# Performance work log

Measured on AMD Instinct MI355X. Metric: run time of the kernel, lower is better.

## Reference

```python
import jax, jax.numpy as jnp
import numpy as np

HIDDEN = 256
HEADS = 8
HEAD_SIZE = HIDDEN // HEADS  # 32
CTX = 512
FF = 4 * HIDDEN
LN_EPS = 1e-5


def setup_inputs() -> dict:
    key = jax.random.key(0)
    ks = jax.random.split(key, 12)
    s = 0.02
    return {
        "x": jax.random.normal(ks[0], (32, CTX, HIDDEN), dtype=jnp.float32),
        # per-head Q/K/V projections, stored [H, D, E] ([in, out] orientation)
        "wq": jax.random.normal(ks[1], (HEADS, HIDDEN, HEAD_SIZE), dtype=jnp.float32) * s,
        "wk": jax.random.normal(ks[2], (HEADS, HIDDEN, HEAD_SIZE), dtype=jnp.float32) * s,
        "wv": jax.random.normal(ks[3], (HEADS, HIDDEN, HEAD_SIZE), dtype=jnp.float32) * s,
        "w_proj": jax.random.normal(ks[4], (HIDDEN, HIDDEN), dtype=jnp.float32) * s,
        "w1": jax.random.normal(ks[5], (HIDDEN, FF), dtype=jnp.float32) * s,
        "b1": jnp.zeros((FF,), dtype=jnp.float32),
        "w2": jax.random.normal(ks[6], (FF, HIDDEN), dtype=jnp.float32) * s,
        "b2": jnp.zeros((HIDDEN,), dtype=jnp.float32),
        "g_ln1": jnp.ones((HIDDEN,), dtype=jnp.float32),
        "be_ln1": jnp.zeros((HIDDEN,), dtype=jnp.float32),
        "g_ln2": jnp.ones((HIDDEN,), dtype=jnp.float32),
        "be_ln2": jnp.zeros((HIDDEN,), dtype=jnp.float32),
    }


def _layernorm(x, g, b):
    mu = jnp.mean(x, axis=-1, keepdims=True)
    var = jnp.var(x, axis=-1, keepdims=True)
    return (x - mu) * jax.lax.rsqrt(var + LN_EPS) * g + b


def reference(x, wq, wk, wv, w_proj, w1, b1, w2, b2, g_ln1, be_ln1, g_ln2, be_ln2):
    B, S, D = x.shape  # S == CTX
    # per-head projections: [B, H, S, E]
    q = jnp.einsum("bsd,hde->bhse", x, wq)
    k = jnp.einsum("bsd,hde->bhse", x, wk)
    v = jnp.einsum("bsd,hde->bhse", x, wv)
    scores = jnp.einsum("bhse,bhte->bhst", q, k) * (HEAD_SIZE ** -0.5)
    causal = jnp.tril(jnp.ones((S, S), dtype=bool))  # [S, S]
    scores = jnp.where(causal, scores, -jnp.inf)
    attn = jax.nn.softmax(scores, axis=-1)
    ctx = jnp.einsum("bhst,bhte->bhse", attn, v)
    ctx = ctx.transpose(0, 2, 1, 3).reshape(B, S, D)  # concat heads
    attn_out = ctx @ w_proj
    h = x + _layernorm(attn_out, g_ln1, be_ln1)
    ff = jax.nn.relu(h @ w1 + b1) @ w2 + b2
    return x + _layernorm(ff, g_ln2, be_ln2)
```

## Files before the change

kernel.cpp:

```cpp
#include <hip/hip_runtime.h>
#include <hip/hip_bf16.h>

#define B_   32
#define S_   512
#define D_   256
#define H_   8
#define E_   32
#define FF_  1024
#define T_   (B_ * S_)

typedef __attribute__((ext_vector_type(8))) short short8;
typedef __attribute__((ext_vector_type(4))) float f32x4;

static __device__ __forceinline__ unsigned short f2bf(float f) {
    union { float f; unsigned int u; } c; c.f = f;
    unsigned int u = c.u;
    u += 0x7fffu + ((u >> 16) & 1u);
    return (unsigned short)(u >> 16);
}
static __device__ __forceinline__ float bf2f(unsigned short u) {
    union { unsigned int u; float f; } c; c.u = ((unsigned int)u) << 16;
    return c.f;
}
static __device__ __forceinline__ unsigned int cvtpk(float lo, float hi) {
    unsigned int r;
    asm("v_cvt_pk_bf16_f32 %0, %1, %2" : "=v"(r) : "v"(lo), "v"(hi));
    return r;
}

#define GLOAD16(g, l) __builtin_amdgcn_global_load_lds( \
    (const __attribute__((address_space(1))) void*)(g), \
    (__attribute__((address_space(3))) void*)(l), 16, 0, 0)

__global__ void prep_kernel(const float* __restrict__ x,
                            const float* __restrict__ wq, const float* __restrict__ wk,
                            const float* __restrict__ wv, const float* __restrict__ w_proj,
                            const float* __restrict__ w1, const float* __restrict__ w2,
                            unsigned short* __restrict__ xb, unsigned short* __restrict__ Wqkv,
                            unsigned short* __restrict__ Wproj, unsigned short* __restrict__ W1t,
                            unsigned short* __restrict__ W2t) {
    int blk = blockIdx.x, tid = threadIdx.x;
    if (blk < 4096) {
        int i = blk * 256 + tid;
        float4 v = *(const float4*)&x[(size_t)i * 4];
        ushort4 o; o.x = f2bf(v.x); o.y = f2bf(v.y); o.z = f2bf(v.z); o.w = f2bf(v.w);
        *(ushort4*)&xb[(size_t)i * 4] = o;
    } else if (blk < 4864) {
        int idx = (blk - 4096) * 256 + tid;
        int nn = idx >> 8, k = idx & 255;
        int which = nn >> 8, r = nn & 255, h = r >> 5, e = r & 31;
        const float* w = (which == 0) ? wq : (which == 1 ? wk : wv);
        float v = w[(h * D_ + k) * E_ + e];
        if (which == 0) v *= 0.17677669529663687f * 1.4426950408889634f;
        Wqkv[idx] = f2bf(v);
    } else if (blk < 5120) {
        int idx = (blk - 4864) * 256 + tid;
        int nn = idx >> 8, k = idx & 255;
        Wproj[idx] = f2bf(w_proj[(size_t)k * 256 + nn]);
    } else if (blk < 6144) {
        int idx = (blk - 5120) * 256 + tid;
        int nn = idx >> 8, k = idx & 255;
        W1t[idx] = f2bf(w1[(size_t)k * 1024 + nn]);
    } else {
        int idx = (blk - 6144) * 256 + tid;
        int nn = idx >> 10, k = idx & 1023;
        W2t[idx] = f2bf(w2[(size_t)k * 256 + nn]);
    }
}

template <int EP, int BN>
__global__ __launch_bounds__(256) void gemm_mfma(const unsigned short* __restrict__ A,
                                                 const unsigned short* __restrict__ Bt,
                                                 const float* __restrict__ bias,
                                                 void* __restrict__ Cout,
                                                 unsigned short* __restrict__ Vout,
                                                 int M, int N, int K) {
    constexpr int FN = BN / 32;
    constexpr int NLD = 2 + BN / 64;
    __shared__ char smem[24576 + BN * 192];
    const int tid = threadIdx.x;
    const int bm = blockIdx.y * 128, bn = blockIdx.x * BN;
    const int wave = tid >> 6, lane = tid & 63;
    const int l15 = lane & 15, kc = lane >> 4;
    const int wr = (wave >> 1) * 64, wc = (wave & 1) * (BN / 2);

    auto waitN = [&]() {
        if constexpr (NLD == 3)      asm volatile("s_waitcnt vmcnt(3)" ::: "memory");
        else if constexpr (NLD == 4) asm volatile("s_waitcnt vmcnt(4)" ::: "memory");
        else                         asm volatile("s_waitcnt vmcnt(6)" ::: "memory");
    };

    auto stage = [&](int buf, int kt) {
        int k0 = kt * 32;
        char* aBase = smem + buf * 8192;
        char* bBase = smem + 24576 + buf * (BN * 64);
        #pragma unroll
        for (int j = 0; j < 2; ++j) {
            int o = j * 256 + tid;
            int r = o >> 2, c = o & 3;
            int g = c ^ ((r >> 1) & 3);
            GLOAD16(A + (size_t)(bm + r) * K + k0 + g * 8, aBase + o * 16);
        }
        #pragma unroll
        for (int j = 0; j < BN / 64; ++j) {
            int o = j * 256 + tid;
            int r = o >> 2, c = o & 3;
            int g = c ^ ((r >> 1) & 3);
            GLOAD16(Bt + (size_t)(bn + r) * K + k0 + g * 8, bBase + o * 16);
        }
    };

    f32x4 acc[4][FN];
    #pragma unroll
    for (int m = 0; m < 4; ++m)
        #pragma unroll
        for (int n = 0; n < FN; ++n) acc[m][n] = (f32x4){0.f, 0.f, 0.f, 0.f};

    const int NT = K >> 5;
    stage(0, 0);
    stage(1, 1);
    waitN();
    __builtin_amdgcn_s_barrier();

    int cur = 0;
    for (int kt = 0; kt < NT; ++kt) {
        const char* aBase = smem + cur * 8192;
        const char* bBase = smem + 24576 + cur * (BN * 64);
        short8 afr[4], bfr[FN];
        #pragma unroll
        for (int m = 0; m < 4; ++m) {
            int row = wr + m * 16 + l15;
            int cc = kc ^ ((row >> 1) & 3);
            afr[m] = *(const short8*)(aBase + row * 64 + cc * 16);
        }
        #pragma unroll
        for (int n = 0; n < FN; ++n) {
            int row = wc + n * 16 + l15;
            int cc = kc ^ ((row >> 1) & 3);
            bfr[n] = *(const short8*)(bBase + row * 64 + cc * 16);
        }
        int nxt2 = cur + 2; if (nxt2 >= 3) nxt2 -= 3;
        if (kt + 2 < NT) stage(nxt2, kt + 2);

        __builtin_amdgcn_s_setprio(1);
        #pragma unroll
        for (int m = 0; m < 4; ++m)
            #pragma unroll
            for (int n = 0; n < FN; ++n)
                acc[m][n] = __builtin_amdgcn_mfma_f32_16x16x32_bf16(afr[m], bfr[n], acc[m][n], 0, 0, 0);
        __builtin_amdgcn_s_setprio(0);

        if (kt + 1 < NT) {
            if (kt + 2 < NT) waitN();
            else asm volatile("s_waitcnt vmcnt(0)" ::: "memory");
            __builtin_amdgcn_s_barrier();
        }
        ++cur; if (cur >= 3) cur -= 3;
    }

    if (EP & 8) {
        #pragma unroll
        for (int n = 0; n < FN; ++n) {
            int col = bn + wc + n * 16 + l15;
            if (col < 512) {
                #pragma unroll
                for (int m = 0; m < 4; ++m) {
                    int row0 = bm + wr + m * 16 + kc * 4;
                    #pragma unroll
                    for (int j = 0; j < 4; ++j)
                        ((unsigned short*)Cout)[(size_t)(row0 + j) * 512 + col] = f2bf(acc[m][n][j]);
                }
            } else {
                int hh = (col - 512) >> 5, e = (col - 512) & 31;
                #pragma unroll
                for (int m = 0; m < 4; ++m) {
                    int row0 = bm + wr + m * 16 + kc * 4;
                    int bb = row0 >> 9, s0 = row0 & 511;
                    ushort4 o4;
                    o4.x = f2bf(acc[m][n][0]); o4.y = f2bf(acc[m][n][1]);
                    o4.z = f2bf(acc[m][n][2]); o4.w = f2bf(acc[m][n][3]);
                    *(ushort4*)&Vout[(size_t)(bb * 8 + hh) * 16384 + e * 512 + s0] = o4;
                }
            }
        }
    } else {
        #pragma unroll
        for (int n = 0; n < FN; ++n) {
            int col = bn + wc + n * 16 + l15;
            float bv = (EP & 1) ? bias[col] : 0.f;
            #pragma unroll
            for (int m = 0; m < 4; ++m) {
                int row0 = bm + wr + m * 16 + kc * 4;
                #pragma unroll
                for (int j = 0; j < 4; ++j) {
                    float v = acc[m][n][j] + bv;
                    if (EP & 2) v = fmaxf(v, 0.f);
                    if (EP & 4) ((unsigned short*)Cout)[(size_t)(row0 + j) * N + col] = f2bf(v);
                    else        ((float*)Cout)[(size_t)(row0 + j) * N + col] = v;
                }
            }
        }
    }
}

template <int BIAS, int OUTF32>
__global__ __launch_bounds__(256) void gemm_ln2(const unsigned short* __restrict__ A,
                                                const unsigned short* __restrict__ Bt,
                                                const float* __restrict__ bias,
                                                const float* __restrict__ xres,
                                                const float* __restrict__ gw,
                                                const float* __restrict__ bw,
                                                void* __restrict__ Cout,
                                                int K) {
    __shared__ char smem[55296];
    __shared__ float sred[2][2][32];
    const int tid = threadIdx.x;
    const int bm = blockIdx.x * 32;
    const int wave = tid >> 6, lane = tid & 63;
    const int l15 = lane & 15, kc = lane >> 4;
    const int wr = (wave >> 1) * 16, wc = (wave & 1) * 128;

    auto stage = [&](int buf, int kt) {
        int k0 = kt * 32;
        char* aBase = smem + buf * 2048;
        char* bBase = smem + 6144 + buf * 16384;
        {
            int o = tid & 127;
            int r = o >> 2, c = o & 3;
            int g = c ^ ((r >> 1) & 3);
            GLOAD16(A + (size_t)(bm + r) * K + k0 + g * 8, aBase + o * 16);
        }
        #pragma unroll
        for (int j = 0; j < 4; ++j) {
            int o = j * 256 + tid;
            int r = o >> 2, c = o & 3;
            int g = c ^ ((r >> 1) & 3);
            GLOAD16(Bt + (size_t)r * K + k0 + g * 8, bBase + o * 16);
        }
    };

    f32x4 acc[8];
    #pragma unroll
    for (int n = 0; n < 8; ++n) acc[n] = (f32x4){0.f, 0.f, 0.f, 0.f};

    const int NT = K >> 5;
    stage(0, 0);
    stage(1, 1);
    asm volatile("s_waitcnt vmcnt(5)" ::: "memory");
    __builtin_amdgcn_s_barrier();

    int cur = 0;
    for (int kt = 0; kt < NT; ++kt) {
        const char* aBase = smem + cur * 2048;
        const char* bBase = smem + 6144 + cur * 16384;
        short8 afr, bfr[8];
        {
            int row = wr + l15;
            int cc = kc ^ ((row >> 1) & 3);
            afr = *(const short8*)(aBase + row * 64 + cc * 16);
        }
        #pragma unroll
        for (int n = 0; n < 8; ++n) {
            int row = wc + n * 16 + l15;
            int cc = kc ^ ((row >> 1) & 3);
            bfr[n] = *(const short8*)(bBase + row * 64 + cc * 16);
        }
        int nxt2 = cur + 2; if (nxt2 >= 3) nxt2 -= 3;
        if (kt + 2 < NT) stage(nxt2, kt + 2);

        __builtin_amdgcn_s_setprio(1);
        #pragma unroll
        for (int n = 0; n < 8; ++n)
            acc[n] = __builtin_amdgcn_mfma_f32_16x16x32_bf16(afr, bfr[n], acc[n], 0, 0, 0);
        __builtin_amdgcn_s_setprio(0);

        if (kt + 1 < NT) {
            if (kt + 2 < NT) asm volatile("s_waitcnt vmcnt(5)" ::: "memory");
            else             asm volatile("s_waitcnt vmcnt(0)" ::: "memory");
            __builtin_amdgcn_s_barrier();
        }
        ++cur; if (cur >= 3) cur -= 3;
    }

    float gv[8], bev[8];
    #pragma unroll
    for (int n = 0; n < 8; ++n) {
        int col = wc + n * 16 + l15;
        gv[n] = gw[col]; bev[n] = bw[col];
        if (BIAS) {
            float bb = bias[col];
            #pragma unroll
            for (int j = 0; j < 4; ++j) acc[n][j] += bb;
        }
    }

    #pragma unroll
    for (int j = 0; j < 4; ++j) {
        float s = 0.f, s2 = 0.f;
        #pragma unroll
        for (int n = 0; n < 8; ++n) { float v = acc[n][j]; s += v; s2 += v * v; }
        #pragma unroll
        for (int off = 1; off < 16; off <<= 1) {
            s += __shfl_xor(s, off); s2 += __shfl_xor(s2, off);
        }
        if (l15 == 0) {
            int rl = wr + kc * 4 + j;
            sred[wave & 1][0][rl] = s;
            sred[wave & 1][1][rl] = s2;
        }
    }
    __syncthreads();

    #pragma unroll
    for (int j = 0; j < 4; ++j) {
        int rl = wr + kc * 4 + j;
        float stot  = sred[0][0][rl] + sred[1][0][rl];
        float s2tot = sred[0][1][rl] + sred[1][1][rl];
        float mu  = stot * (1.f / 256.f);
        float var = s2tot * (1.f / 256.f) - mu * mu;
        float rr  = rsqrtf(var + 1e-5f);
        int rowg = bm + rl;
        #pragma unroll
        for (int n = 0; n < 8; ++n) {
            int col = wc + n * 16 + l15;
            float o = xres[(size_t)rowg * 256 + col] + (acc[n][j] - mu) * rr * gv[n] + bev[n];
            if (OUTF32) ((float*)Cout)[(size_t)rowg * 256 + col] = o;
            else ((unsigned short*)Cout)[(size_t)rowg * 256 + col] = f2bf(o);
        }
    }
}

__global__ __launch_bounds__(512, 1) void attn_mfma(const unsigned short* __restrict__ qk,
                                                    const unsigned short* __restrict__ vtg,
                                                    unsigned short* __restrict__ ctx) {
    __shared__ unsigned short klds[512 * 32];
    __shared__ unsigned short vlds[32 * 512];
    __shared__ unsigned short plds[8][32 * 64];
    const int bh = blockIdx.x;
    const int b = bh >> 3, h = bh & 7;
    const int tid = threadIdx.x;
    const int wave = tid >> 6, lane = tid & 63;
    const int l15 = lane & 15, kc = lane >> 4;

    const unsigned short* kg = qk + (size_t)b * 512 * 512 + 256 + h * 32;
    #pragma unroll
    for (int it = 0; it < 4; ++it) {
        int slot = it * 512 + tid;
        int r = slot >> 2, c = slot & 3;
        GLOAD16(kg + (size_t)r * 512 + (c ^ ((r >> 1) & 3)) * 8, (char*)klds + slot * 16);
    }
    #pragma unroll
    for (int it = 0; it < 4; ++it) {
        int slot = it * 512 + tid;
        int e = slot >> 6, c = slot & 63;
        GLOAD16(vtg + (size_t)bh * 16384 + e * 512 + (c ^ (e & 7)) * 8,
                (char*)vlds + slot * 16);
    }

    const int cA = wave, cB = 15 - wave;
    const int ntA = (cA >> 1) + 1, ntB = (cB >> 1) + 1;
    short8 qfA[2], qfB[2];
    #pragma unroll
    for (int qm = 0; qm < 2; ++qm) {
        qfA[qm] = *(const short8*)(qk + (size_t)(b * 512 + cA * 32 + qm * 16 + l15) * 512 + h * 32 + kc * 8);
        qfB[qm] = *(const short8*)(qk + (size_t)(b * 512 + cB * 32 + qm * 16 + l15) * 512 + h * 32 + kc * 8);
    }
    __syncthreads();

    unsigned short* pw = plds[wave];
    const int xsw = (l15 & 7) << 1;

    f32x4 OA[2][2], OB[2][2];
    float lA[2] = {0.f, 0.f}, lB[2] = {0.f, 0.f};
    #pragma unroll
    for (int qm = 0; qm < 2; ++qm) {
        OA[qm][0] = (f32x4){0.f, 0.f, 0.f, 0.f}; OA[qm][1] = (f32x4){0.f, 0.f, 0.f, 0.f};
        OB[qm][0] = (f32x4){0.f, 0.f, 0.f, 0.f}; OB[qm][1] = (f32x4){0.f, 0.f, 0.f, 0.f};
    }

    auto chunk_step = [&](const short8* qf, f32x4 (&O)[2][2], float* lreg,
                          int cc_, bool diag, const short8* kf, int t0) {
        #pragma unroll
        for (int qm = 0; qm < 2; ++qm) {
            f32x4 st[4];
            __builtin_amdgcn_s_setprio(1);
            #pragma unroll
            for (int tn = 0; tn < 4; ++tn)
                st[tn] = __builtin_amdgcn_mfma_f32_16x16x32_bf16(kf[tn], qf[qm],
                                                                 (f32x4){0.f, 0.f, 0.f, 0.f}, 0, 0, 0);
            __builtin_amdgcn_s_setprio(0);
            if (diag) {
                int qg = cc_ * 32 + qm * 16 + l15;
                #pragma unroll
                for (int tn = 0; tn < 4; ++tn)
                    #pragma unroll
                    for (int j = 0; j < 4; ++j)
                        if (t0 + tn * 16 + kc * 4 + j > qg) st[tn][j] = -1e30f;
            }
            float psum = 0.f;
            #pragma unroll
            for (int tn = 0; tn < 4; ++tn) {
                float p0 = __builtin_amdgcn_exp2f(st[tn][0]);
                float p1 = __builtin_amdgcn_exp2f(st[tn][1]);
                float p2 = __builtin_amdgcn_exp2f(st[tn][2]);
                float p3 = __builtin_amdgcn_exp2f(st[tn][3]);
                psum += (p0 + p1) + (p2 + p3);
                uint2 w;
                w.x = cvtpk(p0, p1);
                w.y = cvtpk(p2, p3);
                int tc = (tn * 4 + kc) ^ xsw;
                *(uint2*)(pw + (qm * 16 + l15) * 64 + tc * 4) = w;
            }
            psum += __shfl_xor(psum, 16);
            psum += __shfl_xor(psum, 32);
            lreg[qm] += psum;
        }
        #pragma unroll
        for (int tt = 0; tt < 2; ++tt) {
            short8 pa[2];
            #pragma unroll
            for (int qm = 0; qm < 2; ++qm) {
                int tcr = (tt * 8 + kc * 2) ^ xsw;
                pa[qm] = *(const short8*)(pw + (qm * 16 + l15) * 64 + tcr * 4);
            }
            short8 vt[2];
            #pragma unroll
            for (int n = 0; n < 2; ++n) {
                int e = n * 16 + l15;
                int c = ((t0 >> 3) + tt * 4 + kc) ^ (e & 7);
                vt[n] = *(const short8*)(vlds + e * 512 + c * 8);
            }
            __builtin_amdgcn_s_setprio(1);
            #pragma unroll
            for (int qm = 0; qm < 2; ++qm)
                #pragma unroll
                for (int n = 0; n < 2; ++n)
                    O[qm][n] = __builtin_amdgcn_mfma_f32_16x16x32_bf16(pa[qm], vt[n], O[qm][n], 0, 0, 0);
            __builtin_amdgcn_s_setprio(0);
        }
    };

    for (int ti = 0; ti < ntB; ++ti) {
        const int t0 = ti * 64;
        short8 kf[4];
        #pragma unroll
        for (int tn = 0; tn < 4; ++tn) {
            int row = t0 + tn * 16 + l15;
            int cx = kc ^ ((row >> 1) & 3);
            kf[tn] = *(const short8*)((const char*)klds + row * 64 + cx * 16);
        }
        if (ti < ntA) chunk_step(qfA, OA, lA, cA, ti == ntA - 1, kf, t0);
        chunk_step(qfB, OB, lB, cB, ti == ntB - 1, kf, t0);
    }

    auto epilogue = [&](f32x4 (&O)[2][2], float* lreg, int cc_) {
        #pragma unroll
        for (int qm = 0; qm < 2; ++qm) {
            float linv = 1.f / lreg[qm];
            #pragma unroll
            for (int j = 0; j < 4; ++j) {
                float lj = __shfl(linv, kc * 4 + j, 16);
                size_t base = (size_t)(b * 512 + cc_ * 32 + qm * 16 + kc * 4 + j) * 256 + h * 32;
                ctx[base + l15]      = f2bf(O[qm][0][j] * lj);
                ctx[base + 16 + l15] = f2bf(O[qm][1][j] * lj);
            }
        }
    };
    epilogue(OA, lA, cA);
    epilogue(OB, lB, cB);
}

extern "C" void kernel_launch(void* const* d_in, const int* in_sizes, int n_in,
                              void* d_out, int out_size, void* d_ws, size_t ws_size,
                              hipStream_t stream) {
    (void)in_sizes; (void)n_in; (void)out_size; (void)ws_size;
    const float* x      = (const float*)d_in[0];
    const float* wq     = (const float*)d_in[1];
    const float* wk     = (const float*)d_in[2];
    const float* wv     = (const float*)d_in[3];
    const float* w_proj = (const float*)d_in[4];
    const float* w1     = (const float*)d_in[5];
    const float* b1     = (const float*)d_in[6];
    const float* w2     = (const float*)d_in[7];
    const float* b2     = (const float*)d_in[8];
    const float* g1     = (const float*)d_in[9];
    const float* be1    = (const float*)d_in[10];
    const float* g2     = (const float*)d_in[11];
    const float* be2    = (const float*)d_in[12];
    float* out = (float*)d_out;

    char* W = (char*)d_ws;
    unsigned short* qk      = (unsigned short*)(W + 0);
    unsigned short* vtg     = (unsigned short*)(W + 16777216);
    unsigned short* xb      = (unsigned short*)(W + 25165824);
    unsigned short* ctx     = (unsigned short*)(W + 25165824);
    unsigned short* hbuf    = (unsigned short*)(W + 33554432);
    unsigned short* ff1     = (unsigned short*)(W + 0);
    unsigned short* Wqkv_t  = (unsigned short*)(W + 50331648);
    unsigned short* Wproj_t = (unsigned short*)(W + 50724864);
    unsigned short* W1_t    = (unsigned short*)(W + 50855936);
    unsigned short* W2_t    = (unsigned short*)(W + 51380224);

    prep_kernel<<<7168, 256, 0, stream>>>(x, wq, wk, wv, w_proj, w1, w2,
                                          xb, Wqkv_t, Wproj_t, W1_t, W2_t);

    gemm_mfma<8, 128><<<dim3(6, T_ / 128), 256, 0, stream>>>(xb, Wqkv_t, nullptr, qk, vtg, T_, 768, 256);

    attn_mfma<<<B_ * H_, 512, 0, stream>>>(qk, vtg, ctx);

    gemm_ln2<0, 0><<<T_ / 32, 256, 0, stream>>>(ctx, Wproj_t, nullptr, x, g1, be1, hbuf, 256);

    gemm_mfma<7, 256><<<dim3(FF_ / 256, T_ / 128), 256, 0, stream>>>(hbuf, W1_t, b1, ff1, nullptr, T_, FF_, 256);

    gemm_ln2<1, 1><<<T_ / 32, 256, 0, stream>>>(ff1, W2_t, b2, x, g2, be2, out, 1024);
}
```

Before: 102.7 us.

## Widen MFMA GEMM blocks to 8 waves with 256-row tiles

```diff
diff --git a/kernel.cpp b/kernel.cpp
--- a/kernel.cpp
+++ b/kernel.cpp
@@ -69,44 +69,52 @@
 }
 
 template <int EP, int BN>
-__global__ __launch_bounds__(256) void gemm_mfma(const unsigned short* __restrict__ A,
-                                                 const unsigned short* __restrict__ Bt,
-                                                 const float* __restrict__ bias,
-                                                 void* __restrict__ Cout,
-                                                 unsigned short* __restrict__ Vout,
-                                                 int M, int N, int K) {
+__global__ __launch_bounds__(512, 2) void gemm_mfma8(const unsigned short* __restrict__ A,
+                                                     const unsigned short* __restrict__ Bt,
+                                                     const float* __restrict__ bias,
+                                                     void* __restrict__ Cout,
+                                                     unsigned short* __restrict__ Vout,
+                                                     int M, int N, int K) {
     constexpr int FN = BN / 32;
-    constexpr int NLD = 2 + BN / 64;
-    __shared__ char smem[24576 + BN * 192];
+    __shared__ char smem[49152 + BN * 192];
     const int tid = threadIdx.x;
-    const int bm = blockIdx.y * 128, bn = blockIdx.x * BN;
+    const int bm = blockIdx.y * 256, bn = blockIdx.x * BN;
     const int wave = tid >> 6, lane = tid & 63;
     const int l15 = lane & 15, kc = lane >> 4;
-    const int wr = (wave >> 1) * 64, wc = (wave & 1) * (BN / 2);
-
-    auto waitN = [&]() {
-        if constexpr (NLD == 3)      asm volatile("s_waitcnt vmcnt(3)" ::: "memory");
-        else if constexpr (NLD == 4) asm volatile("s_waitcnt vmcnt(4)" ::: "memory");
-        else                         asm volatile("s_waitcnt vmcnt(6)" ::: "memory");
-    };
+    const int wr = (wave & 3) * 64, wc = (wave >> 2) * (BN / 2);
 
     auto stage = [&](int buf, int kt) {
         int k0 = kt * 32;
-        char* aBase = smem + buf * 8192;
-        char* bBase = smem + 24576 + buf * (BN * 64);
+        char* aBase = smem + buf * 16384;
+        char* bBase = smem + 49152 + buf * (BN * 64);
         #pragma unroll
         for (int j = 0; j < 2; ++j) {
-            int o = j * 256 + tid;
+            int o = j * 512 + tid;
             int r = o >> 2, c = o & 3;
             int g = c ^ ((r >> 1) & 3);
             GLOAD16(A + (size_t)(bm + r) * K + k0 + g * 8, aBase + o * 16);
         }
-        #pragma unroll
-        for (int j = 0; j < BN / 64; ++j) {
-            int o = j * 256 + tid;
-            int r = o >> 2, c = o & 3;
-            int g = c ^ ((r >> 1) & 3);
-            GLOAD16(Bt + (size_t)(bn + r) * K + k0 + g * 8, bBase + o * 16);
+        if constexpr (BN == 256) {
+            #pragma unroll
+            for (int j = 0; j < 2; ++j) {
+                int o = j * 512 + tid;
+                int r = o >> 2, c = o & 3;
+                int g = c ^ ((r >> 1) & 3);
+                GLOAD16(Bt + (size_t)(bn + r) * K + k0 + g * 8, bBase + o * 16);
+            }
+        } else {
+            {
+                int o = tid;
+                int r = o >> 2, c = o & 3;
+                int g = c ^ ((r >> 1) & 3);
+                GLOAD16(Bt + (size_t)(bn + r) * K + k0 + g * 8, bBase + o * 16);
+            }
+            {
+                int o = 512 + (tid & 255);
+                int r = o >> 2, c = o & 3;
+                int g = c ^ ((r >> 1) & 3);
+                GLOAD16(Bt + (size_t)(bn + r) * K + k0 + g * 8, bBase + o * 16);
+            }
         }
     };
 
@@ -119,13 +127,13 @@
     const int NT = K >> 5;
     stage(0, 0);
     stage(1, 1);
-    waitN();
+    asm volatile("s_waitcnt vmcnt(4)" ::: "memory");
     __builtin_amdgcn_s_barrier();
 
     int cur = 0;
     for (int kt = 0; kt < NT; ++kt) {
-        const char* aBase = smem + cur * 8192;
-        const char* bBase = smem + 24576 + cur * (BN * 64);
+        const char* aBase = smem + cur * 16384;
+        const char* bBase = smem + 49152 + cur * (BN * 64);
         short8 afr[4], bfr[FN];
         #pragma unroll
         for (int m = 0; m < 4; ++m) {
@@ -151,8 +159,8 @@
         __builtin_amdgcn_s_setprio(0);
 
         if (kt + 1 < NT) {
-            if (kt + 2 < NT) waitN();
-            else asm volatile("s_waitcnt vmcnt(0)" ::: "memory");
+            if (kt + 2 < NT) asm volatile("s_waitcnt vmcnt(4)" ::: "memory");
+            else             asm volatile("s_waitcnt vmcnt(0)" ::: "memory");
             __builtin_amdgcn_s_barrier();
         }
         ++cur; if (cur >= 3) cur -= 3;
@@ -504,13 +512,13 @@
     prep_kernel<<<7168, 256, 0, stream>>>(x, wq, wk, wv, w_proj, w1, w2,
                                           xb, Wqkv_t, Wproj_t, W1_t, W2_t);
 
-    gemm_mfma<8, 128><<<dim3(6, T_ / 128), 256, 0, stream>>>(xb, Wqkv_t, nullptr, qk, vtg, T_, 768, 256);
+    gemm_mfma8<8, 192><<<dim3(4, T_ / 256), 512, 0, stream>>>(xb, Wqkv_t, nullptr, qk, vtg, T_, 768, 256);
 
     attn_mfma<<<B_ * H_, 512, 0, stream>>>(qk, vtg, ctx);
 
     gemm_ln2<0, 0><<<T_ / 32, 256, 0, stream>>>(ctx, Wproj_t, nullptr, x, g1, be1, hbuf, 256);
 
-    gemm_mfma<7, 256><<<dim3(FF_ / 256, T_ / 128), 256, 0, stream>>>(hbuf, W1_t, b1, ff1, nullptr, T_, FF_, 256);
+    gemm_mfma8<7, 256><<<dim3(FF_ / 256, T_ / 256), 512, 0, stream>>>(hbuf, W1_t, b1, ff1, nullptr, T_, FF_, 256);
 
     gemm_ln2<1, 1><<<T_ / 32, 256, 0, stream>>>(ff1, W2_t, b2, x, g2, be2, out, 1024);
 }
```

Measured after the change: 101.9 us, median of 3. Within noise of the previous version (-0.8%).
